# Performance work log

Measured on AMD Instinct MI355X. Metric: run time of the kernel, lower is better.

The kernel has to match this reference:

```python
import jax, jax.numpy as jnp
import numpy as np

# Production-scale dims (see shape_source)
N = 100000      # nodes
E = 1600000     # shortest-path edges
I = 128         # in_channels
O = 128         # out_channels
K = 5           # max_distance
BN_EPS = 1e-5
GIN_EPS = 0.0   # eps=0.0, trainable_eps=False


def setup_inputs() -> dict:
    key = jax.random.key(0)
    ks = jax.random.split(key, 10)
    node_embeddings = jax.random.normal(ks[0], (N, I), dtype=jnp.float32)
    edge_index = jax.random.randint(ks[1], (2, E), 0, N)          # [2, E] row/col
    edge_weights = jax.random.randint(ks[2], (E,), 1, K + 1)      # SP distance in 1..K
    hop_coef = jax.random.normal(ks[3], (K,), dtype=jnp.float32)
    W1 = jax.random.normal(ks[4], (I, O), dtype=jnp.float32) / np.sqrt(I).astype(np.float32)
    b1 = jnp.zeros((O,), jnp.float32)
    gamma1 = jnp.ones((O,), jnp.float32)
    beta1 = jnp.zeros((O,), jnp.float32)
    W2 = jax.random.normal(ks[5], (O, O), dtype=jnp.float32) / np.sqrt(O).astype(np.float32)
    b2 = jnp.zeros((O,), jnp.float32)
    gamma2 = jnp.ones((O,), jnp.float32)
    beta2 = jnp.zeros((O,), jnp.float32)
    return {
        "node_embeddings": node_embeddings,
        "edge_index": edge_index,
        "edge_weights": edge_weights,
        "hop_coef": hop_coef,
        "W1": W1, "b1": b1, "gamma1": gamma1, "beta1": beta1,
        "W2": W2, "b2": b2, "gamma2": gamma2, "beta2": beta2,
    }


def _batch_norm(x, gamma, beta):
    # BatchNorm1d in training mode: batch mean, biased batch variance
    mean = x.mean(axis=0)
    var = x.var(axis=0)
    return gamma * (x - mean) * jax.lax.rsqrt(var + BN_EPS) + beta


def reference(node_embeddings, edge_index, edge_weights, hop_coef,
              W1, b1, gamma1, beta1, W2, b2, gamma2, beta2):
    # Fused form of the per-hop loop: each edge with SP distance d contributes
    # softmax(hop_coef)[d-1] * x[col] to out[row]. Identical math to K separate
    # sparse.mm's weighted by hop_weights and summed.
    hop_w = jax.nn.softmax(hop_coef)                               # [K]
    valid = (edge_weights >= 1) & (edge_weights <= K)
    w_e = jnp.where(valid, hop_w[jnp.clip(edge_weights - 1, 0, K - 1)], 0.0)  # [E]
    row, col = edge_index[0], edge_index[1]
    msgs = w_e[:, None] * node_embeddings[col]                     # [E, I] gather
    agg = jnp.zeros_like(node_embeddings).at[row].add(msgs)        # [N, I] scatter-add
    h = (1.0 + GIN_EPS) * node_embeddings + agg                    # GIN combine
    h = jax.nn.relu(_batch_norm(h @ W1 + b1, gamma1, beta1))
    h = jax.nn.relu(_batch_norm(h @ W2 + b2, gamma2, beta2))
    return h
```

## Files before the change

kernel.cpp:

```cpp
#include <hip/hip_runtime.h>
#include <hip/hip_bf16.h>


typedef __attribute__((ext_vector_type(8))) short short8;
typedef __attribute__((ext_vector_type(4))) float f32x4;

__device__ inline unsigned short f2bf(float v) {
    unsigned int u = __float_as_uint(v);
    unsigned int r = (u + 0x7fffu + ((u >> 16) & 1u)) >> 16;
    return (unsigned short)r;
}
__device__ inline float bf2f(unsigned int u) {
    return __uint_as_float(u << 16);
}

__global__ __launch_bounds__(256) void prep_k(const float* __restrict__ hc,
        float* __restrict__ hwp, float* __restrict__ sums,
        const float* __restrict__ W1, const float* __restrict__ W2,
        unsigned short* __restrict__ w1h, unsigned short* __restrict__ w1l,
        unsigned short* __restrict__ w2h, unsigned short* __restrict__ w2l,
        int* __restrict__ cnt, const float4* __restrict__ x4,
        uint4* __restrict__ xb, int N, int K, int NBC, long long n8) {
    int b = blockIdx.x, tid = threadIdx.x;
    if (b == 0) {
        sums[tid] = 0.f; sums[tid + 256] = 0.f;
        if (tid == 0) {
            float tmp[8];
            float m = -1e30f;
            for (int k = 0; k < K; ++k) m = fmaxf(m, hc[k]);
            float s = 0.f;
            for (int k = 0; k < K; ++k) { float e = __expf(hc[k] - m); tmp[k] = e; s += e; }
            float inv = 1.f / s;
            for (int k = 0; k < 8; ++k) hwp[k] = 0.f;
            for (int k = 0; k < K; ++k) hwp[k + 1] = tmp[k] * inv;
        }
        return;
    }
    if (b <= 2) {
        const float* W = (b == 2) ? W2 : W1;
        unsigned short* th = (b == 2) ? w2h : w1h;
        unsigned short* tl = (b == 2) ? w2l : w1l;
        for (int i = tid; i < 16384; i += 256) {
            int k = i >> 7, n = i & 127;
            float v = W[k * 128 + n];
            unsigned short hi = f2bf(v);
            th[n * 128 + k] = hi;
            tl[n * 128 + k] = f2bf(v - bf2f(hi));
        }
        return;
    }
    if (b < 3 + NBC) {
        int i = (b - 3) * 256 + tid;
        if (i < N) cnt[i] = 0;
        return;
    }
    long long g = (long long)(b - 3 - NBC) * 256 + tid;
    if (g >= n8) return;
    float4 a = x4[g * 2], c = x4[g * 2 + 1];
    union { unsigned short us[8]; uint4 v; } o;
    o.us[0] = f2bf(a.x); o.us[1] = f2bf(a.y); o.us[2] = f2bf(a.z); o.us[3] = f2bf(a.w);
    o.us[4] = f2bf(c.x); o.us[5] = f2bf(c.y); o.us[6] = f2bf(c.z); o.us[7] = f2bf(c.w);
    xb[g] = o.v;
}

__global__ __launch_bounds__(256) void count_k(const int* __restrict__ rows,
        int* __restrict__ cnt, int* __restrict__ seq, int E) {
    int g = blockIdx.x * 256 + threadIdx.x;
    int e0 = g * 4;
    if (e0 + 4 <= E) {
        int4 r = ((const int4*)rows)[g];
        int4 s;
        s.x = atomicAdd(&cnt[r.x], 1);
        s.y = atomicAdd(&cnt[r.y], 1);
        s.z = atomicAdd(&cnt[r.z], 1);
        s.w = atomicAdd(&cnt[r.w], 1);
        ((int4*)seq)[g] = s;
    } else {
        for (int e = e0; e < E; ++e) seq[e] = atomicAdd(&cnt[rows[e]], 1);
    }
}

__global__ __launch_bounds__(256) void scan1_k(const int* __restrict__ cnt,
        int* __restrict__ s1, int* __restrict__ bsum, int N) {
    __shared__ int lds[256];
    int t = threadIdx.x;
    int i = blockIdx.x * 256 + t;
    int v = (i < N) ? cnt[i] : 0;
    lds[t] = v;
    __syncthreads();
#pragma unroll
    for (int off = 1; off < 256; off <<= 1) {
        int a = lds[t];
        int b = (t >= off) ? lds[t - off] : 0;
        __syncthreads();
        lds[t] = a + b;
        __syncthreads();
    }
    if (i < N) s1[i] = lds[t] - v;
    if (t == 255) bsum[blockIdx.x] = lds[255];
}

__global__ __launch_bounds__(512) void scan2_k(const int* __restrict__ bsum,
        int* __restrict__ bscan, int NB) {
    __shared__ int lds[512];
    int t = threadIdx.x;
    int v = (t < NB) ? bsum[t] : 0;
    lds[t] = v;
    __syncthreads();
#pragma unroll
    for (int off = 1; off < 512; off <<= 1) {
        int a = lds[t];
        int b = (t >= off) ? lds[t - off] : 0;
        __syncthreads();
        lds[t] = a + b;
        __syncthreads();
    }
    if (t < NB) bscan[t] = lds[t] - v;
}

__global__ __launch_bounds__(256) void fill_k(const int* __restrict__ rows,
        const int* __restrict__ cols, const int* __restrict__ ew,
        const int* __restrict__ seq, const int* __restrict__ s1,
        const int* __restrict__ bscan, const float* __restrict__ hwp,
        int2* __restrict__ epay, int E, int K) {
    int g = blockIdx.x * 256 + threadIdx.x;
    int e0 = g * 4;
    if (e0 + 4 <= E) {
        int4 r = ((const int4*)rows)[g];
        int4 c = ((const int4*)cols)[g];
        int4 d = ((const int4*)ew)[g];
        int4 s = ((const int4*)seq)[g];
        int dd;
        dd = (d.x < 1 || d.x > K) ? 0 : d.x;
        epay[s1[r.x] + bscan[r.x >> 8] + s.x] = make_int2(c.x, __float_as_int(hwp[dd]));
        dd = (d.y < 1 || d.y > K) ? 0 : d.y;
        epay[s1[r.y] + bscan[r.y >> 8] + s.y] = make_int2(c.y, __float_as_int(hwp[dd]));
        dd = (d.z < 1 || d.z > K) ? 0 : d.z;
        epay[s1[r.z] + bscan[r.z >> 8] + s.z] = make_int2(c.z, __float_as_int(hwp[dd]));
        dd = (d.w < 1 || d.w > K) ? 0 : d.w;
        epay[s1[r.w] + bscan[r.w >> 8] + s.w] = make_int2(c.w, __float_as_int(hwp[dd]));
    } else {
        for (int e = e0; e < E; ++e) {
            int d = ew[e];
            if (d < 1 || d > K) d = 0;
            int r = rows[e];
            epay[s1[r] + bscan[r >> 8] + seq[e]] = make_int2(cols[e], __float_as_int(hwp[d]));
        }
    }
}

__global__ __launch_bounds__(256) void gather_k(
        const unsigned short* __restrict__ xb, const int2* __restrict__ epay,
        const int* __restrict__ s1, const int* __restrict__ bscan,
        const int* __restrict__ cnt, unsigned short* __restrict__ h, int N) {
    int wid = (blockIdx.x * 256 + threadIdx.x) >> 6;
    if (wid >= N) return;
    int lane = threadIdx.x & 63;
    int half = lane >> 5, li = lane & 31;
    int start = __builtin_amdgcn_readfirstlane(s1[wid] + bscan[wid >> 8]);
    int deg = __builtin_amdgcn_readfirstlane(cnt[wid]);
    const int2* ep = epay + start;
    float a0 = 0.f, a1 = 0.f, a2 = 0.f, a3 = 0.f;
    if (half == 0) {
        uint2 u = *(const uint2*)(xb + (size_t)wid * 128 + li * 4);
        a0 = bf2f(u.x & 0xFFFF); a1 = bf2f(u.x >> 16);
        a2 = bf2f(u.y & 0xFFFF); a3 = bf2f(u.y >> 16);
    }
    int j = 0;
    for (; j + 8 <= deg; j += 8) {
        int2 p0 = ep[j + 0 + half];
        int2 p1 = ep[j + 2 + half];
        int2 p2 = ep[j + 4 + half];
        int2 p3 = ep[j + 6 + half];
        uint2 u0 = *(const uint2*)(xb + (size_t)p0.x * 128 + li * 4);
        uint2 u1 = *(const uint2*)(xb + (size_t)p1.x * 128 + li * 4);
        uint2 u2 = *(const uint2*)(xb + (size_t)p2.x * 128 + li * 4);
        uint2 u3 = *(const uint2*)(xb + (size_t)p3.x * 128 + li * 4);
        float w0 = __int_as_float(p0.y), w1 = __int_as_float(p1.y);
        float w2 = __int_as_float(p2.y), w3 = __int_as_float(p3.y);
        a0 = fmaf(w0, bf2f(u0.x & 0xFFFF), a0); a1 = fmaf(w0, bf2f(u0.x >> 16), a1);
        a2 = fmaf(w0, bf2f(u0.y & 0xFFFF), a2); a3 = fmaf(w0, bf2f(u0.y >> 16), a3);
        a0 = fmaf(w1, bf2f(u1.x & 0xFFFF), a0); a1 = fmaf(w1, bf2f(u1.x >> 16), a1);
        a2 = fmaf(w1, bf2f(u1.y & 0xFFFF), a2); a3 = fmaf(w1, bf2f(u1.y >> 16), a3);
        a0 = fmaf(w2, bf2f(u2.x & 0xFFFF), a0); a1 = fmaf(w2, bf2f(u2.x >> 16), a1);
        a2 = fmaf(w2, bf2f(u2.y & 0xFFFF), a2); a3 = fmaf(w2, bf2f(u2.y >> 16), a3);
        a0 = fmaf(w3, bf2f(u3.x & 0xFFFF), a0); a1 = fmaf(w3, bf2f(u3.x >> 16), a1);
        a2 = fmaf(w3, bf2f(u3.y & 0xFFFF), a2); a3 = fmaf(w3, bf2f(u3.y >> 16), a3);
    }
    for (; j + 2 <= deg; j += 2) {
        int2 p = ep[j + half];
        float w = __int_as_float(p.y);
        uint2 u = *(const uint2*)(xb + (size_t)p.x * 128 + li * 4);
        a0 = fmaf(w, bf2f(u.x & 0xFFFF), a0); a1 = fmaf(w, bf2f(u.x >> 16), a1);
        a2 = fmaf(w, bf2f(u.y & 0xFFFF), a2); a3 = fmaf(w, bf2f(u.y >> 16), a3);
    }
    if (j < deg) {
        int2 p = ep[j];
        float w = half ? 0.f : __int_as_float(p.y);
        uint2 u = *(const uint2*)(xb + (size_t)p.x * 128 + li * 4);
        a0 = fmaf(w, bf2f(u.x & 0xFFFF), a0); a1 = fmaf(w, bf2f(u.x >> 16), a1);
        a2 = fmaf(w, bf2f(u.y & 0xFFFF), a2); a3 = fmaf(w, bf2f(u.y >> 16), a3);
    }
    a0 += __shfl_xor(a0, 32); a1 += __shfl_xor(a1, 32);
    a2 += __shfl_xor(a2, 32); a3 += __shfl_xor(a3, 32);
    if (half == 0) {
        uint2 o;
        o.x = (unsigned int)f2bf(a0) | ((unsigned int)f2bf(a1) << 16);
        o.y = (unsigned int)f2bf(a2) | ((unsigned int)f2bf(a3) << 16);
        *(uint2*)(h + (size_t)wid * 128 + li * 4) = o;
    }
}

template<bool AFFINE>
__global__ __launch_bounds__(256) void gemm_mfma_k(
        const unsigned short* __restrict__ Ain,
        const unsigned short* __restrict__ Bhg, const unsigned short* __restrict__ Blg,
        const float* __restrict__ bias,
        const float* __restrict__ sum_in, const float* __restrict__ sq_in,
        const float* __restrict__ gamma, const float* __restrict__ beta,
        unsigned short* __restrict__ zout,
        float* __restrict__ sum_out, float* __restrict__ sq_out,
        int N, float invN) {
    __shared__ unsigned short Bh[128 * 136];
    __shared__ unsigned short Bl[128 * 136];
    __shared__ float sc_s[128], sh_s[128];
    int tid = threadIdx.x;
    if (AFFINE && tid < 128) {
        float mean = sum_in[tid] * invN;
        float var = fmaxf(sq_in[tid] * invN - mean * mean, 0.f);
        float s = gamma[tid] * rsqrtf(var + 1e-5f);
        sc_s[tid] = s;
        sh_s[tid] = beta[tid] - mean * s;
    }
    for (int i = tid; i < 4096; i += 256) {
        int halfb = i >> 11;
        int j = i & 2047;
        int n = j >> 4, c = j & 15;
        const uint4* src = (const uint4*)((halfb ? Blg : Bhg) + n * 128 + c * 8);
        uint4* dst = (uint4*)((halfb ? Bl : Bh) + n * 136 + c * 8);
        *dst = *src;
    }
    __syncthreads();

    int wave = tid >> 6, lane = tid & 63;
    int n16 = lane & 15, q = lane >> 4;
    int rowbase = blockIdx.x * 128 + wave * 32;

    f32x4 acc[2][8];
#pragma unroll
    for (int mt = 0; mt < 2; mt++)
#pragma unroll
        for (int t = 0; t < 8; t++) acc[mt][t] = (f32x4){0.f, 0.f, 0.f, 0.f};

    int ldsb = n16 * 136 + q * 8;

#pragma unroll
    for (int k0 = 0; k0 < 128; k0 += 32) {
        short8 afr[2];
        float4 s0, s1v, t0, t1;
        if (AFFINE) {
            s0 = *(const float4*)&sc_s[k0 + q * 8];
            s1v = *(const float4*)&sc_s[k0 + q * 8 + 4];
            t0 = *(const float4*)&sh_s[k0 + q * 8];
            t1 = *(const float4*)&sh_s[k0 + q * 8 + 4];
        }
#pragma unroll
        for (int mt = 0; mt < 2; mt++) {
            int ar = rowbase + mt * 16 + n16;
            ar = min(ar, N - 1);
            size_t off = (size_t)ar * 128 + k0 + q * 8;
            short8 raw = *(const short8*)(Ain + off);
            if (!AFFINE) {
                afr[mt] = raw;
            } else {
                float v[8];
                v[0] = fmaxf(fmaf(bf2f((unsigned short)raw[0]), s0.x, t0.x), 0.f);
                v[1] = fmaxf(fmaf(bf2f((unsigned short)raw[1]), s0.y, t0.y), 0.f);
                v[2] = fmaxf(fmaf(bf2f((unsigned short)raw[2]), s0.z, t0.z), 0.f);
                v[3] = fmaxf(fmaf(bf2f((unsigned short)raw[3]), s0.w, t0.w), 0.f);
                v[4] = fmaxf(fmaf(bf2f((unsigned short)raw[4]), s1v.x, t1.x), 0.f);
                v[5] = fmaxf(fmaf(bf2f((unsigned short)raw[5]), s1v.y, t1.y), 0.f);
                v[6] = fmaxf(fmaf(bf2f((unsigned short)raw[6]), s1v.z, t1.z), 0.f);
                v[7] = fmaxf(fmaf(bf2f((unsigned short)raw[7]), s1v.w, t1.w), 0.f);
#pragma unroll
                for (int e = 0; e < 8; e++) afr[mt][e] = (short)f2bf(v[e]);
            }
        }
#pragma unroll
        for (int t = 0; t < 8; t++) {
            short8 bhi = *(const short8*)&Bh[t * 16 * 136 + ldsb + k0];
            short8 blo = *(const short8*)&Bl[t * 16 * 136 + ldsb + k0];
#pragma unroll
            for (int mt = 0; mt < 2; mt++) {
                acc[mt][t] = __builtin_amdgcn_mfma_f32_16x16x32_bf16(afr[mt], bhi, acc[mt][t], 0, 0, 0);
                acc[mt][t] = __builtin_amdgcn_mfma_f32_16x16x32_bf16(afr[mt], blo, acc[mt][t], 0, 0, 0);
            }
        }
    }

    float csum[8], csq[8];
#pragma unroll
    for (int t = 0; t < 8; t++) { csum[t] = 0.f; csq[t] = 0.f; }
#pragma unroll
    for (int t = 0; t < 8; t++) {
        int col = n16 + 16 * t;
        float bv = bias[col];
#pragma unroll
        for (int mt = 0; mt < 2; mt++) {
#pragma unroll
            for (int r = 0; r < 4; r++) {
                int row = rowbase + mt * 16 + q * 4 + r;
                if (row < N) {
                    float v = acc[mt][t][r] + bv;
                    zout[(size_t)row * 128 + col] = f2bf(v);
                    csum[t] += v;
                    csq[t] += v * v;
                }
            }
        }
    }
#pragma unroll
    for (int t = 0; t < 8; t++) {
        csum[t] += __shfl_xor(csum[t], 16);
        csum[t] += __shfl_xor(csum[t], 32);
        csq[t] += __shfl_xor(csq[t], 16);
        csq[t] += __shfl_xor(csq[t], 32);
    }
    __syncthreads();
    float* red = (float*)Bh;
    if (q == 0) {
#pragma unroll
        for (int t = 0; t < 8; t++) {
            int col = n16 + 16 * t;
            red[wave * 128 + col] = csum[t];
            red[512 + wave * 128 + col] = csq[t];
        }
    }
    __syncthreads();
    if (tid < 128) {
        float s = 0.f, qq = 0.f;
#pragma unroll
        for (int w = 0; w < 4; w++) {
            s += red[w * 128 + tid];
            qq += red[512 + w * 128 + tid];
        }
        unsafeAtomicAdd(&sum_out[tid], s);
        unsafeAtomicAdd(&sq_out[tid], qq);
    }
}

__global__ __launch_bounds__(256) void apply_k(const unsigned short* __restrict__ z2,
        const float* __restrict__ sum2, const float* __restrict__ sq2,
        const float* __restrict__ gamma, const float* __restrict__ beta,
        float* __restrict__ out, long long n8, float invN) {
    __shared__ float sc[128], sh[128];
    int tid = threadIdx.x;
    if (tid < 128) {
        float mean = sum2[tid] * invN;
        float var = fmaxf(sq2[tid] * invN - mean * mean, 0.f);
        float s = gamma[tid] * rsqrtf(var + 1e-5f);
        sc[tid] = s;
        sh[tid] = beta[tid] - mean * s;
    }
    __syncthreads();
    long long g = (long long)blockIdx.x * 256 + tid;
    if (g >= n8) return;
    uint4 u = ((const uint4*)z2)[g];
    int cb = (int)((g * 8) & 127);
    float4 s0 = *(const float4*)&sc[cb], s1 = *(const float4*)&sc[cb + 4];
    float4 t0 = *(const float4*)&sh[cb], t1 = *(const float4*)&sh[cb + 4];
    float4 o0, o1;
    o0.x = fmaxf(fmaf(bf2f(u.x & 0xFFFF), s0.x, t0.x), 0.f);
    o0.y = fmaxf(fmaf(bf2f(u.x >> 16), s0.y, t0.y), 0.f);
    o0.z = fmaxf(fmaf(bf2f(u.y & 0xFFFF), s0.z, t0.z), 0.f);
    o0.w = fmaxf(fmaf(bf2f(u.y >> 16), s0.w, t0.w), 0.f);
    o1.x = fmaxf(fmaf(bf2f(u.z & 0xFFFF), s1.x, t1.x), 0.f);
    o1.y = fmaxf(fmaf(bf2f(u.z >> 16), s1.y, t1.y), 0.f);
    o1.z = fmaxf(fmaf(bf2f(u.w & 0xFFFF), s1.z, t1.z), 0.f);
    o1.w = fmaxf(fmaf(bf2f(u.w >> 16), s1.w, t1.w), 0.f);
    ((float4*)out)[g * 2] = o0;
    ((float4*)out)[g * 2 + 1] = o1;
}

extern "C" void kernel_launch(void* const* d_in, const int* in_sizes, int n_in,
                              void* d_out, int out_size, void* d_ws, size_t ws_size,
                              hipStream_t stream) {
    const float* x   = (const float*)d_in[0];
    const int*   ei  = (const int*)d_in[1];
    const int*   ew  = (const int*)d_in[2];
    const float* hc  = (const float*)d_in[3];
    const float* W1  = (const float*)d_in[4];
    const float* b1  = (const float*)d_in[5];
    const float* g1  = (const float*)d_in[6];
    const float* be1 = (const float*)d_in[7];
    const float* W2  = (const float*)d_in[8];
    const float* b2  = (const float*)d_in[9];
    const float* g2  = (const float*)d_in[10];
    const float* be2 = (const float*)d_in[11];

    int N = in_sizes[0] / 128;
    int E = in_sizes[2];
    int K = in_sizes[3];
    int NB = (N + 255) / 256;
    size_t NF = (size_t)N * 128;
    long long n8 = (long long)(NF / 8);

    unsigned short* h = (unsigned short*)d_ws;
    unsigned short* xb = h + NF;
    unsigned short* z1 = xb;
    unsigned short* z2 = h;
    int2* epay = (int2*)(xb + NF);
    int* cnt = (int*)(epay + E);
    int* s1 = cnt + N;
    int* bscan = s1 + N;
    int* bsum = bscan + 512;
    int* seq = bsum + 512;
    unsigned short* w1h = (unsigned short*)(seq + E);
    unsigned short* w1l = w1h + 16384;
    unsigned short* w2h = w1l + 16384;
    unsigned short* w2l = w2h + 16384;
    float* hwp = (float*)(w2l + 16384);
    float* sums = hwp + 8;
    float* sum1 = sums, *sq1 = sums + 128, *sum2 = sums + 256, *sq2 = sums + 384;

    float invN = 1.0f / (float)N;

    {
        int NX = (int)((n8 + 255) / 256);
        prep_k<<<3 + NB + NX, 256, 0, stream>>>(hc, hwp, sums, W1, W2,
            w1h, w1l, w2h, w2l, cnt, (const float4*)x, (uint4*)xb, N, K, NB, n8);
    }
    {
        int blocks = (E / 4 + 256) / 256;
        count_k<<<blocks, 256, 0, stream>>>(ei, cnt, seq, E);
    }
    scan1_k<<<NB, 256, 0, stream>>>(cnt, s1, bsum, N);
    scan2_k<<<1, 512, 0, stream>>>(bsum, bscan, NB);
    {
        int blocks = (E / 4 + 256) / 256;
        fill_k<<<blocks, 256, 0, stream>>>(ei, ei + E, ew, seq, s1, bscan, hwp, epay, E, K);
    }
    {
        long long tot = (long long)N * 64;
        gather_k<<<(int)((tot + 255) / 256), 256, 0, stream>>>(xb, epay, s1, bscan,
            cnt, h, N);
    }
    int gblocks = (N + 127) / 128;
    gemm_mfma_k<false><<<gblocks, 256, 0, stream>>>(h, w1h, w1l, b1,
        nullptr, nullptr, nullptr, nullptr, z1, sum1, sq1, N, invN);
    gemm_mfma_k<true><<<gblocks, 256, 0, stream>>>(z1, w2h, w2l, b2,
        sum1, sq1, g1, be1, z2, sum2, sq2, N, invN);
    apply_k<<<(int)((n8 + 255) / 256), 256, 0, stream>>>(z2, sum2, sq2, g2, be2,
        (float*)d_out, n8, invN);
}
```

Before: 460.2 us.

## Merge count into prep, widen gather edge loads, split BN1 out of GEMM

The edge-count atomics move into the prep kernel, and the count buffer is cleared with a memset instead of prep blocks. The gather loop now handles 16 edges per iteration using int4 payload loads, and the bf16 unpacking is simplified. The GEMM drops its AFFINE template and stages the hi and lo weight halves through a single LDS buffer in turn, which halves LDS use and targets higher occupancy. BN1 becomes a separate elementwise kernel, which adds a launch and one extra pass over memory in exchange for a simpler GEMM.

```diff
diff --git a/kernel.cpp b/kernel.cpp
--- a/kernel.cpp
+++ b/kernel.cpp
@@ -7,21 +7,38 @@
 
 __device__ inline unsigned short f2bf(float v) {
     unsigned int u = __float_as_uint(v);
-    unsigned int r = (u + 0x7fffu + ((u >> 16) & 1u)) >> 16;
-    return (unsigned short)r;
-}
-__device__ inline float bf2f(unsigned int u) {
-    return __uint_as_float(u << 16);
-}
-
-__global__ __launch_bounds__(256) void prep_k(const float* __restrict__ hc,
-        float* __restrict__ hwp, float* __restrict__ sums,
+    return (unsigned short)((u + 0x7fffu + ((u >> 16) & 1u)) >> 16);
+}
+__device__ inline float bf2f(unsigned int u) { return __uint_as_float(u << 16); }
+__device__ inline float bflo(unsigned int u) { return __uint_as_float(u << 16); }
+__device__ inline float bfhi(unsigned int u) { return __uint_as_float(u & 0xFFFF0000u); }
+
+__global__ __launch_bounds__(256) void prep_k(
+        const int* __restrict__ rows, int* __restrict__ cnt, int* __restrict__ seq,
+        int E, int NE4,
+        const float* __restrict__ hc, float* __restrict__ hwp, float* __restrict__ sums,
         const float* __restrict__ W1, const float* __restrict__ W2,
         unsigned short* __restrict__ w1h, unsigned short* __restrict__ w1l,
         unsigned short* __restrict__ w2h, unsigned short* __restrict__ w2l,
-        int* __restrict__ cnt, const float4* __restrict__ x4,
-        uint4* __restrict__ xb, int N, int K, int NBC, long long n8) {
+        const float4* __restrict__ x4, uint4* __restrict__ xb, int K, long long n8) {
     int b = blockIdx.x, tid = threadIdx.x;
+    if (b < NE4) {
+        int g = b * 256 + tid;
+        int e0 = g * 4;
+        if (e0 + 4 <= E) {
+            int4 r = ((const int4*)rows)[g];
+            int4 s;
+            s.x = atomicAdd(&cnt[r.x], 1);
+            s.y = atomicAdd(&cnt[r.y], 1);
+            s.z = atomicAdd(&cnt[r.z], 1);
+            s.w = atomicAdd(&cnt[r.w], 1);
+            ((int4*)seq)[g] = s;
+        } else {
+            for (int e = e0; e < E; ++e) seq[e] = atomicAdd(&cnt[rows[e]], 1);
+        }
+        return;
+    }
+    b -= NE4;
     if (b == 0) {
         sums[tid] = 0.f; sums[tid + 256] = 0.f;
         if (tid == 0) {
@@ -49,35 +66,13 @@
         }
         return;
     }
-    if (b < 3 + NBC) {
-        int i = (b - 3) * 256 + tid;
-        if (i < N) cnt[i] = 0;
-        return;
-    }
-    long long g = (long long)(b - 3 - NBC) * 256 + tid;
+    long long g = (long long)(b - 3) * 256 + tid;
     if (g >= n8) return;
     float4 a = x4[g * 2], c = x4[g * 2 + 1];
     union { unsigned short us[8]; uint4 v; } o;
     o.us[0] = f2bf(a.x); o.us[1] = f2bf(a.y); o.us[2] = f2bf(a.z); o.us[3] = f2bf(a.w);
     o.us[4] = f2bf(c.x); o.us[5] = f2bf(c.y); o.us[6] = f2bf(c.z); o.us[7] = f2bf(c.w);
     xb[g] = o.v;
-}
-
-__global__ __launch_bounds__(256) void count_k(const int* __restrict__ rows,
-        int* __restrict__ cnt, int* __restrict__ seq, int E) {
-    int g = blockIdx.x * 256 + threadIdx.x;
-    int e0 = g * 4;
-    if (e0 + 4 <= E) {
-        int4 r = ((const int4*)rows)[g];
-        int4 s;
-        s.x = atomicAdd(&cnt[r.x], 1);
-        s.y = atomicAdd(&cnt[r.y], 1);
-        s.z = atomicAdd(&cnt[r.z], 1);
-        s.w = atomicAdd(&cnt[r.w], 1);
-        ((int4*)seq)[g] = s;
-    } else {
-        for (int e = e0; e < E; ++e) seq[e] = atomicAdd(&cnt[rows[e]], 1);
-    }
 }
 
 __global__ __launch_bounds__(256) void scan1_k(const int* __restrict__ cnt,
@@ -160,46 +155,41 @@
     int start = __builtin_amdgcn_readfirstlane(s1[wid] + bscan[wid >> 8]);
     int deg = __builtin_amdgcn_readfirstlane(cnt[wid]);
     const int2* ep = epay + start;
+    const unsigned short* xrow = xb + li * 4;
     float a0 = 0.f, a1 = 0.f, a2 = 0.f, a3 = 0.f;
     if (half == 0) {
         uint2 u = *(const uint2*)(xb + (size_t)wid * 128 + li * 4);
-        a0 = bf2f(u.x & 0xFFFF); a1 = bf2f(u.x >> 16);
-        a2 = bf2f(u.y & 0xFFFF); a3 = bf2f(u.y >> 16);
+        a0 = bflo(u.x); a1 = bfhi(u.x);
+        a2 = bflo(u.y); a3 = bfhi(u.y);
     }
     int j = 0;
-    for (; j + 8 <= deg; j += 8) {
-        int2 p0 = ep[j + 0 + half];
-        int2 p1 = ep[j + 2 + half];
-        int2 p2 = ep[j + 4 + half];
-        int2 p3 = ep[j + 6 + half];
-        uint2 u0 = *(const uint2*)(xb + (size_t)p0.x * 128 + li * 4);
-        uint2 u1 = *(const uint2*)(xb + (size_t)p1.x * 128 + li * 4);
-        uint2 u2 = *(const uint2*)(xb + (size_t)p2.x * 128 + li * 4);
-        uint2 u3 = *(const uint2*)(xb + (size_t)p3.x * 128 + li * 4);
-        float w0 = __int_as_float(p0.y), w1 = __int_as_float(p1.y);
-        float w2 = __int_as_float(p2.y), w3 = __int_as_float(p3.y);
-        a0 = fmaf(w0, bf2f(u0.x & 0xFFFF), a0); a1 = fmaf(w0, bf2f(u0.x >> 16), a1);
-        a2 = fmaf(w0, bf2f(u0.y & 0xFFFF), a2); a3 = fmaf(w0, bf2f(u0.y >> 16), a3);
-        a0 = fmaf(w1, bf2f(u1.x & 0xFFFF), a0); a1 = fmaf(w1, bf2f(u1.x >> 16), a1);
-        a2 = fmaf(w1, bf2f(u1.y & 0xFFFF), a2); a3 = fmaf(w1, bf2f(u1.y >> 16), a3);
-        a0 = fmaf(w2, bf2f(u2.x & 0xFFFF), a0); a1 = fmaf(w2, bf2f(u2.x >> 16), a1);
-        a2 = fmaf(w2, bf2f(u2.y & 0xFFFF), a2); a3 = fmaf(w2, bf2f(u2.y >> 16), a3);
-        a0 = fmaf(w3, bf2f(u3.x & 0xFFFF), a0); a1 = fmaf(w3, bf2f(u3.x >> 16), a1);
-        a2 = fmaf(w3, bf2f(u3.y & 0xFFFF), a2); a3 = fmaf(w3, bf2f(u3.y >> 16), a3);
+    for (; j + 16 <= deg; j += 16) {
+        int4 qv[8];
+#pragma unroll
+        for (int i = 0; i < 8; i++) qv[i] = *(const int4*)&ep[j + 2 * i];
+#pragma unroll
+        for (int i = 0; i < 8; i++) {
+            int c = half ? qv[i].z : qv[i].x;
+            float w = __int_as_float(half ? qv[i].w : qv[i].y);
+            uint2 u = *(const uint2*)(xrow + (size_t)c * 128);
+            a0 = fmaf(w, bflo(u.x), a0); a1 = fmaf(w, bfhi(u.x), a1);
+            a2 = fmaf(w, bflo(u.y), a2); a3 = fmaf(w, bfhi(u.y), a3);
+        }
     }
     for (; j + 2 <= deg; j += 2) {
-        int2 p = ep[j + half];
-        float w = __int_as_float(p.y);
-        uint2 u = *(const uint2*)(xb + (size_t)p.x * 128 + li * 4);
-        a0 = fmaf(w, bf2f(u.x & 0xFFFF), a0); a1 = fmaf(w, bf2f(u.x >> 16), a1);
-        a2 = fmaf(w, bf2f(u.y & 0xFFFF), a2); a3 = fmaf(w, bf2f(u.y >> 16), a3);
+        int4 qv = *(const int4*)&ep[j];
+        int c = half ? qv.z : qv.x;
+        float w = __int_as_float(half ? qv.w : qv.y);
+        uint2 u = *(const uint2*)(xrow + (size_t)c * 128);
+        a0 = fmaf(w, bflo(u.x), a0); a1 = fmaf(w, bfhi(u.x), a1);
+        a2 = fmaf(w, bflo(u.y), a2); a3 = fmaf(w, bfhi(u.y), a3);
     }
     if (j < deg) {
         int2 p = ep[j];
         float w = half ? 0.f : __int_as_float(p.y);
-        uint2 u = *(const uint2*)(xb + (size_t)p.x * 128 + li * 4);
-        a0 = fmaf(w, bf2f(u.x & 0xFFFF), a0); a1 = fmaf(w, bf2f(u.x >> 16), a1);
-        a2 = fmaf(w, bf2f(u.y & 0xFFFF), a2); a3 = fmaf(w, bf2f(u.y >> 16), a3);
+        uint2 u = *(const uint2*)(xrow + (size_t)p.x * 128);
+        a0 = fmaf(w, bflo(u.x), a0); a1 = fmaf(w, bfhi(u.x), a1);
+        a2 = fmaf(w, bflo(u.y), a2); a3 = fmaf(w, bfhi(u.y), a3);
     }
     a0 += __shfl_xor(a0, 32); a1 += __shfl_xor(a1, 32);
     a2 += __shfl_xor(a2, 32); a3 += __shfl_xor(a3, 32);
@@ -211,92 +201,62 @@
     }
 }
 
-template<bool AFFINE>
-__global__ __launch_bounds__(256) void gemm_mfma_k(
+__global__ __launch_bounds__(256, 4) void gemm_mfma_k(
         const unsigned short* __restrict__ Ain,
         const unsigned short* __restrict__ Bhg, const unsigned short* __restrict__ Blg,
-        const float* __restrict__ bias,
-        const float* __restrict__ sum_in, const float* __restrict__ sq_in,
-        const float* __restrict__ gamma, const float* __restrict__ beta,
-        unsigned short* __restrict__ zout,
-        float* __restrict__ sum_out, float* __restrict__ sq_out,
-        int N, float invN) {
-    __shared__ unsigned short Bh[128 * 136];
-    __shared__ unsigned short Bl[128 * 136];
-    __shared__ float sc_s[128], sh_s[128];
+        const float* __restrict__ bias, unsigned short* __restrict__ zout,
+        float* __restrict__ sum_out, float* __restrict__ sq_out, int N) {
+    __shared__ unsigned short Bs[128 * 136];
     int tid = threadIdx.x;
-    if (AFFINE && tid < 128) {
-        float mean = sum_in[tid] * invN;
-        float var = fmaxf(sq_in[tid] * invN - mean * mean, 0.f);
-        float s = gamma[tid] * rsqrtf(var + 1e-5f);
-        sc_s[tid] = s;
-        sh_s[tid] = beta[tid] - mean * s;
-    }
-    for (int i = tid; i < 4096; i += 256) {
-        int halfb = i >> 11;
-        int j = i & 2047;
-        int n = j >> 4, c = j & 15;
-        const uint4* src = (const uint4*)((halfb ? Blg : Bhg) + n * 128 + c * 8);
-        uint4* dst = (uint4*)((halfb ? Bl : Bh) + n * 136 + c * 8);
-        *dst = *src;
-    }
-    __syncthreads();
-
     int wave = tid >> 6, lane = tid & 63;
     int n16 = lane & 15, q = lane >> 4;
     int rowbase = blockIdx.x * 128 + wave * 32;
 
-    f32x4 acc[2][8];
-#pragma unroll
-    for (int mt = 0; mt < 2; mt++)
-#pragma unroll
-        for (int t = 0; t < 8; t++) acc[mt][t] = (f32x4){0.f, 0.f, 0.f, 0.f};
-
-    int ldsb = n16 * 136 + q * 8;
-
-#pragma unroll
-    for (int k0 = 0; k0 < 128; k0 += 32) {
-        short8 afr[2];
-        float4 s0, s1v, t0, t1;
-        if (AFFINE) {
-            s0 = *(const float4*)&sc_s[k0 + q * 8];
-            s1v = *(const float4*)&sc_s[k0 + q * 8 + 4];
-            t0 = *(const float4*)&sh_s[k0 + q * 8];
-            t1 = *(const float4*)&sh_s[k0 + q * 8 + 4];
-        }
+    for (int i = tid; i < 2048; i += 256) {
+        int n = i >> 4, c = i & 15;
+        *(uint4*)&Bs[n * 136 + c * 8] = *(const uint4*)(Bhg + n * 128 + c * 8);
+    }
+
+    short8 afr[4][2];
+#pragma unroll
+    for (int kk = 0; kk < 4; kk++)
 #pragma unroll
         for (int mt = 0; mt < 2; mt++) {
             int ar = rowbase + mt * 16 + n16;
             ar = min(ar, N - 1);
-            size_t off = (size_t)ar * 128 + k0 + q * 8;
-            short8 raw = *(const short8*)(Ain + off);
-            if (!AFFINE) {
-                afr[mt] = raw;
-            } else {
-                float v[8];
-                v[0] = fmaxf(fmaf(bf2f((unsigned short)raw[0]), s0.x, t0.x), 0.f);
-                v[1] = fmaxf(fmaf(bf2f((unsigned short)raw[1]), s0.y, t0.y), 0.f);
-                v[2] = fmaxf(fmaf(bf2f((unsigned short)raw[2]), s0.z, t0.z), 0.f);
-                v[3] = fmaxf(fmaf(bf2f((unsigned short)raw[3]), s0.w, t0.w), 0.f);
-                v[4] = fmaxf(fmaf(bf2f((unsigned short)raw[4]), s1v.x, t1.x), 0.f);
-                v[5] = fmaxf(fmaf(bf2f((unsigned short)raw[5]), s1v.y, t1.y), 0.f);
-                v[6] = fmaxf(fmaf(bf2f((unsigned short)raw[6]), s1v.z, t1.z), 0.f);
-                v[7] = fmaxf(fmaf(bf2f((unsigned short)raw[7]), s1v.w, t1.w), 0.f);
-#pragma unroll
-                for (int e = 0; e < 8; e++) afr[mt][e] = (short)f2bf(v[e]);
-            }
-        }
+            afr[kk][mt] = *(const short8*)(Ain + (size_t)ar * 128 + kk * 32 + q * 8);
+        }
+
+    f32x4 acc[2][8];
+#pragma unroll
+    for (int mt = 0; mt < 2; mt++)
+#pragma unroll
+        for (int t = 0; t < 8; t++) acc[mt][t] = (f32x4){0.f, 0.f, 0.f, 0.f};
+
+    __syncthreads();
+    int ldsb = n16 * 136 + q * 8;
+#pragma unroll
+    for (int kk = 0; kk < 4; kk++)
 #pragma unroll
         for (int t = 0; t < 8; t++) {
-            short8 bhi = *(const short8*)&Bh[t * 16 * 136 + ldsb + k0];
-            short8 blo = *(const short8*)&Bl[t * 16 * 136 + ldsb + k0];
-#pragma unroll
-            for (int mt = 0; mt < 2; mt++) {
-                acc[mt][t] = __builtin_amdgcn_mfma_f32_16x16x32_bf16(afr[mt], bhi, acc[mt][t], 0, 0, 0);
-                acc[mt][t] = __builtin_amdgcn_mfma_f32_16x16x32_bf16(afr[mt], blo, acc[mt][t], 0, 0, 0);
-            }
-        }
-    }
+            short8 b = *(const short8*)&Bs[t * 16 * 136 + ldsb + kk * 32];
+            acc[0][t] = __builtin_amdgcn_mfma_f32_16x16x32_bf16(afr[kk][0], b, acc[0][t], 0, 0, 0);
+            acc[1][t] = __builtin_amdgcn_mfma_f32_16x16x32_bf16(afr[kk][1], b, acc[1][t], 0, 0, 0);
+        }
+    __syncthreads();
+    for (int i = tid; i < 2048; i += 256) {
+        int n = i >> 4, c = i & 15;
+        *(uint4*)&Bs[n * 136 + c * 8] = *(const uint4*)(Blg + n * 128 + c * 8);
+    }
+    __syncthreads();
+#pragma unroll
+    for (int kk = 0; kk < 4; kk++)
+#pragma unroll
+        for (int t = 0; t < 8; t++) {
+            short8 b = *(const short8*)&Bs[t * 16 * 136 + ldsb + kk * 32];
+            acc[0][t] = __builtin_amdgcn_mfma_f32_16x16x32_bf16(afr[kk][0], b, acc[0][t], 0, 0, 0);
+            acc[1][t] = __builtin_amdgcn_mfma_f32_16x16x32_bf16(afr[kk][1], b, acc[1][t], 0, 0, 0);
+        }
 
     float csum[8], csq[8];
 #pragma unroll
@@ -327,7 +287,7 @@
         csq[t] += __shfl_xor(csq[t], 32);
     }
     __syncthreads();
-    float* red = (float*)Bh;
+    float* red = (float*)Bs;
     if (q == 0) {
 #pragma unroll
         for (int t = 0; t < 8; t++) {
@@ -349,7 +309,43 @@
     }
 }
 
-__global__ __launch_bounds__(256) void apply_k(const unsigned short* __restrict__ z2,
+__global__ __launch_bounds__(256) void bn1_k(const uint4* __restrict__ z,
+        const float* __restrict__ sum, const float* __restrict__ sq,
+        const float* __restrict__ gamma, const float* __restrict__ beta,
+        uint4* __restrict__ out, long long n8, float invN) {
+    __shared__ float sc[128], sh[128];
+    int tid = threadIdx.x;
+    if (tid < 128) {
+        float mean = sum[tid] * invN;
+        float var = fmaxf(sq[tid] * invN - mean * mean, 0.f);
+        float s = gamma[tid] * rsqrtf(var + 1e-5f);
+        sc[tid] = s;
+        sh[tid] = beta[tid] - mean * s;
+    }
+    __syncthreads();
+    long long g = (long long)blockIdx.x * 256 + tid;
+    if (g >= n8) return;
+    uint4 u = z[g];
+    int cb = (int)((g * 8) & 127);
+    float4 s0 = *(const float4*)&sc[cb], s1 = *(const float4*)&sc[cb + 4];
+    float4 t0 = *(const float4*)&sh[cb], t1 = *(const float4*)&sh[cb + 4];
+    float v0 = fmaxf(fmaf(bflo(u.x), s0.x, t0.x), 0.f);
+    float v1 = fmaxf(fmaf(bfhi(u.x), s0.y, t0.y), 0.f);
+    float v2 = fmaxf(fmaf(bflo(u.y), s0.z, t0.z), 0.f);
+    float v3 = fmaxf(fmaf(bfhi(u.y), s0.w, t0.w), 0.f);
+    float v4 = fmaxf(fmaf(bflo(u.z), s1.x, t1.x), 0.f);
+    float v5 = fmaxf(fmaf(bfhi(u.z), s1.y, t1.y), 0.f);
+    float v6 = fmaxf(fmaf(bflo(u.w), s1.z, t1.z), 0.f);
+    float v7 = fmaxf(fmaf(bfhi(u.w), s1.w, t1.w), 0.f);
+    uint4 o;
+    o.x = (unsigned int)f2bf(v0) | ((unsigned int)f2bf(v1) << 16);
+    o.y = (unsigned int)f2bf(v2) | ((unsigned int)f2bf(v3) << 16);
+    o.z = (unsigned int)f2bf(v4) | ((unsigned int)f2bf(v5) << 16);
+    o.w = (unsigned int)f2bf(v6) | ((unsigned int)f2bf(v7) << 16);
+    out[g] = o;
+}
+
+__global__ __launch_bounds__(256) void bn2_k(const unsigned short* __restrict__ z2,
         const float* __restrict__ sum2, const float* __restrict__ sq2,
         const float* __restrict__ gamma, const float* __restrict__ beta,
         float* __restrict__ out, long long n8, float invN) {
@@ -370,14 +366,14 @@
     float4 s0 = *(const float4*)&sc[cb], s1 = *(const float4*)&sc[cb + 4];
     float4 t0 = *(const float4*)&sh[cb], t1 = *(const float4*)&sh[cb + 4];
     float4 o0, o1;
-    o0.x = fmaxf(fmaf(bf2f(u.x & 0xFFFF), s0.x, t0.x), 0.f);
-    o0.y = fmaxf(fmaf(bf2f(u.x >> 16), s0.y, t0.y), 0.f);
-    o0.z = fmaxf(fmaf(bf2f(u.y & 0xFFFF), s0.z, t0.z), 0.f);
-    o0.w = fmaxf(fmaf(bf2f(u.y >> 16), s0.w, t0.w), 0.f);
-    o1.x = fmaxf(fmaf(bf2f(u.z & 0xFFFF), s1.x, t1.x), 0.f);
-    o1.y = fmaxf(fmaf(bf2f(u.z >> 16), s1.y, t1.y), 0.f);
-    o1.z = fmaxf(fmaf(bf2f(u.w & 0xFFFF), s1.z, t1.z), 0.f);
-    o1.w = fmaxf(fmaf(bf2f(u.w >> 16), s1.w, t1.w), 0.f);
+    o0.x = fmaxf(fmaf(bflo(u.x), s0.x, t0.x), 0.f);
+    o0.y = fmaxf(fmaf(bfhi(u.x), s0.y, t0.y), 0.f);
+    o0.z = fmaxf(fmaf(bflo(u.y), s0.z, t0.z), 0.f);
+    o0.w = fmaxf(fmaf(bfhi(u.y), s0.w, t0.w), 0.f);
+    o1.x = fmaxf(fmaf(bflo(u.z), s1.x, t1.x), 0.f);
+    o1.y = fmaxf(fmaf(bfhi(u.z), s1.y, t1.y), 0.f);
+    o1.z = fmaxf(fmaf(bflo(u.w), s1.z, t1.z), 0.f);
+    o1.w = fmaxf(fmaf(bfhi(u.w), s1.w, t1.w), 0.f);
     ((float4*)out)[g * 2] = o0;
     ((float4*)out)[g * 2 + 1] = o1;
 }
@@ -402,20 +398,23 @@
     int E = in_sizes[2];
     int K = in_sizes[3];
     int NB = (N + 255) / 256;
+    int NE4 = (E / 4 + 255) / 256 + 1;
     size_t NF = (size_t)N * 128;
     long long n8 = (long long)(NF / 8);
+    int NX = (int)((n8 + 255) / 256);
 
     unsigned short* h = (unsigned short*)d_ws;
     unsigned short* xb = h + NF;
     unsigned short* z1 = xb;
-    unsigned short* z2 = h;
+    unsigned short* a1 = h;
+    unsigned short* z2 = xb;
     int2* epay = (int2*)(xb + NF);
     int* cnt = (int*)(epay + E);
     int* s1 = cnt + N;
     int* bscan = s1 + N;
     int* bsum = bscan + 512;
     int* seq = bsum + 512;
-    unsigned short* w1h = (unsigned short*)(seq + E);
+    unsigned short* w1h = (unsigned short*)(seq + E + 4);
     unsigned short* w1l = w1h + 16384;
     unsigned short* w2h = w1l + 16384;
     unsigned short* w2l = w2h + 16384;
@@ -425,31 +424,23 @@
 
     float invN = 1.0f / (float)N;
 
-    {
-        int NX = (int)((n8 + 255) / 256);
-        prep_k<<<3 + NB + NX, 256, 0, stream>>>(hc, hwp, sums, W1, W2,
-            w1h, w1l, w2h, w2l, cnt, (const float4*)x, (uint4*)xb, N, K, NB, n8);
-    }
-    {
-        int blocks = (E / 4 + 256) / 256;
-        count_k<<<blocks, 256, 0, stream>>>(ei, cnt, seq, E);
-    }
+    hipMemsetAsync(cnt, 0, (size_t)N * sizeof(int), stream);
+
+    prep_k<<<NE4 + 3 + NX, 256, 0, stream>>>(ei, cnt, seq, E, NE4,
+        hc, hwp, sums, W1, W2, w1h, w1l, w2h, w2l,
+        (const float4*)x, (uint4*)xb, K, n8);
     scan1_k<<<NB, 256, 0, stream>>>(cnt, s1, bsum, N);
     scan2_k<<<1, 512, 0, stream>>>(bsum, bscan, NB);
-    {
-        int blocks = (E / 4 + 256) / 256;
-        fill_k<<<blocks, 256, 0, stream>>>(ei, ei + E, ew, seq, s1, bscan, hwp, epay, E, K);
-    }
+    fill_k<<<NE4, 256, 0, stream>>>(ei, ei + E, ew, seq, s1, bscan, hwp, epay, E, K);
     {
         long long tot = (long long)N * 64;
         gather_k<<<(int)((tot + 255) / 256), 256, 0, stream>>>(xb, epay, s1, bscan,
             cnt, h, N);
     }
     int gblocks = (N + 127) / 128;
-    gemm_mfma_k<false><<<gblocks, 256, 0, stream>>>(h, w1h, w1l, b1,
-        nullptr, nullptr, nullptr, nullptr, z1, sum1, sq1, N, invN);
-    gemm_mfma_k<true><<<gblocks, 256, 0, stream>>>(z1, w2h, w2l, b2,
-        sum1, sq1, g1, be1, z2, sum2, sq2, N, invN);
-    apply_k<<<(int)((n8 + 255) / 256), 256, 0, stream>>>(z2, sum2, sq2, g2, be2,
-        (float*)d_out, n8, invN);
-}
+    gemm_mfma_k<<<gblocks, 256, 0, stream>>>(h, w1h, w1l, b1, z1, sum1, sq1, N);
+    bn1_k<<<NX, 256, 0, stream>>>((const uint4*)z1, sum1, sq1, g1, be1,
+        (uint4*)a1, n8, invN);
+    gemm_mfma_k<<<gblocks, 256, 0, stream>>>(a1, w2h, w2l, b2, z2, sum2, sq2, N);
+    bn2_k<<<NX, 256, 0, stream>>>(z2, sum2, sq2, g2, be2, (float*)d_out, n8, invN);
+}
```

Measured after the change: 531.9 us. 15.6% more time.
